# Kernel optimization log

Measured on AMD Instinct MI355X. Metric: run time of the kernel, lower is better.

## Reference

```python
import jax, jax.numpy as jnp
import numpy as np

EPS = 1e-7  # K.epsilon()
ROUTINGS = 3

def squash(v, axis=-1):
    s2 = jnp.sum(jnp.square(v), axis=axis, keepdims=True)
    scale = s2 / (1.0 + s2) / jnp.sqrt(s2 + EPS)
    return scale * v

def setup_inputs() -> dict:
    key = jax.random.key(0)
    k1, k2 = jax.random.split(key)
    B, N, I = 128, 512, 256   # batch, input_num_capsule, input_dim_capsule
    M, D = 32, 16             # num_capsule, dim_capsule
    x = jax.random.normal(k1, (B, N, I), dtype=jnp.float32)
    W = jax.random.normal(k2, (M, N, D, I), dtype=jnp.float32) * 0.05
    return {"x": x, "W": W}

def reference(x, W):
    # x: [B,N,I], W: [M,N,D,I]
    # inputs_hat[b,m,n,d] = sum_i x[b,n,i] * W[m,n,d,i]
    inputs_hat = jnp.einsum('bni,mndi->bmnd', x, W)
    B, M, N, _ = inputs_hat.shape
    b = jnp.zeros((B, M, N), dtype=inputs_hat.dtype)
    outputs = None
    for i in range(ROUTINGS):
        c = jax.nn.softmax(b, axis=1)  # softmax over num_capsule dim (dim=1)
        s = jnp.einsum('bmn,bmnd->bmd', c, inputs_hat)
        outputs = squash(s)
        if i < ROUTINGS - 1:
            b = b + jnp.einsum('bmd,bmnd->bmn', outputs, inputs_hat)
    return outputs
```

## Files before the change

kernel.cpp:

```cpp
#include <hip/hip_runtime.h>
#include <stdint.h>

#define B_ 128
#define N_ 512
#define I_ 256
#define M_ 32
#define D_ 16

typedef __attribute__((ext_vector_type(4))) float f32x4;
typedef __attribute__((ext_vector_type(4))) float float4v;
typedef __attribute__((ext_vector_type(8))) short short8;
typedef __attribute__((ext_vector_type(4))) unsigned int u32x4;
typedef __attribute__((ext_vector_type(4))) unsigned short ushort4v;
typedef unsigned short ushort;

__device__ __forceinline__ float bf2f(ushort u) {
    union { unsigned int i; float f; } v; v.i = ((unsigned int)u) << 16; return v.f;
}
__device__ __forceinline__ ushort f2bf(float f) {
    union { float f; unsigned int i; } v; v.f = f;
    unsigned int r = v.i + 0x7FFFu + ((v.i >> 16) & 1u);
    return (ushort)(r >> 16);
}

__device__ __forceinline__ short8 cvt8(float4v lo, float4v hi) {
    unsigned int u0, u1, u2, u3;
    asm("v_cvt_pk_bf16_f32 %0, %1, %2" : "=v"(u0) : "v"(lo[0]), "v"(lo[1]));
    asm("v_cvt_pk_bf16_f32 %0, %1, %2" : "=v"(u1) : "v"(lo[2]), "v"(lo[3]));
    asm("v_cvt_pk_bf16_f32 %0, %1, %2" : "=v"(u2) : "v"(hi[0]), "v"(hi[1]));
    asm("v_cvt_pk_bf16_f32 %0, %1, %2" : "=v"(u3) : "v"(hi[2]), "v"(hi[3]));
    u32x4 uv = {u0, u1, u2, u3};
    return __builtin_bit_cast(short8, uv);
}

#define GL16(dst, base, imm) \
    asm volatile("global_load_dwordx4 %0, %1, off offset:%2" \
                 : "=&v"(dst) : "v"(base), "n"(imm))

#define VMW(nn) do { \
    asm volatile("s_waitcnt vmcnt(" #nn ")" ::: "memory"); \
    __builtin_amdgcn_sched_barrier(0); \
} while (0)

__global__ __launch_bounds__(512, 4) void hat_gemm(const float* __restrict__ x,
                                                   const float* __restrict__ W,
                                                   ushort* __restrict__ hat) {
    __shared__ ushort As[128 * 256];

    const int bid = blockIdx.x;
    const int n   = (bid & 7) * 64 + (bid >> 3);

    const int tid  = threadIdx.x;
    const int lane = tid & 63;
    const int w    = tid >> 6;
    const int l15  = lane & 15;
    const int kq   = lane >> 4;

    {
        const int row = tid >> 2;
        const int seg = tid & 3;
        const float* xp = x + ((size_t)row * N_ + n) * I_ + seg * 64;
        float4v sv[16];
        #pragma unroll
        for (int j = 0; j < 16; ++j) GL16(sv[j], xp, j * 16);
        VMW(0);
        #pragma unroll
        for (int i = 0; i < 8; ++i) {
            short8 h = cvt8(sv[2 * i], sv[2 * i + 1]);
            const int gsw = ((seg * 8 + i) ^ (row & 15));
            *(short8*)&As[row * 256 + gsw * 8] = h;
        }
    }
    __syncthreads();

    const int abase = l15 * 256;

    #define MF(bb, ks) do { \
        const int gsw_ = (((ks) * 4 + kq) ^ l15) * 8; \
        _Pragma("unroll") \
        for (int a = 0; a < 8; ++a) { \
            short8 af = *(const short8*)&As[abase + a * 4096 + gsw_]; \
            acc[a] = __builtin_amdgcn_mfma_f32_16x16x32_bf16(af, (bb), acc[a], 0, 0, 0); \
        } \
    } while (0)

    #pragma unroll
    for (int mq = 0; mq < 4; ++mq) {
        const int m = w * 4 + mq;
        const float* wm = W + (((size_t)m * N_ + n) * D_ + l15) * I_ + kq * 8;

        f32x4 acc[8];
        #pragma unroll
        for (int a = 0; a < 8; ++a) { f32x4 z = {0.f, 0.f, 0.f, 0.f}; acc[a] = z; }

        float4v L0, H0, L1, H1, L2, H2, L3, H3;
        GL16(L0, wm, 0);   GL16(H0, wm, 16);
        GL16(L1, wm, 128); GL16(H1, wm, 144);
        GL16(L2, wm, 256); GL16(H2, wm, 272);
        GL16(L3, wm, 384); GL16(H3, wm, 400);

        VMW(6); { short8 bb = cvt8(L0, H0); GL16(L0, wm, 512); GL16(H0, wm, 528); MF(bb, 0); }
        VMW(6); { short8 bb = cvt8(L1, H1); GL16(L1, wm, 640); GL16(H1, wm, 656); MF(bb, 1); }
        VMW(6); { short8 bb = cvt8(L2, H2); GL16(L2, wm, 768); GL16(H2, wm, 784); MF(bb, 2); }
        VMW(6); { short8 bb = cvt8(L3, H3); GL16(L3, wm, 896); GL16(H3, wm, 912); MF(bb, 3); }
        VMW(6); { short8 bb = cvt8(L0, H0); MF(bb, 4); }
        VMW(4); { short8 bb = cvt8(L1, H1); MF(bb, 5); }
        VMW(2); { short8 bb = cvt8(L2, H2); MF(bb, 6); }
        VMW(0); { short8 bb = cvt8(L3, H3); MF(bb, 7); }

        #pragma unroll
        for (int a = 0; a < 8; ++a) {
            #pragma unroll
            for (int r = 0; r < 4; ++r) {
                const int brow = a * 16 + kq * 4 + r;
                const size_t idx = (((size_t)brow * M_ + m) * N_ + n) * D_ + l15;
                hat[idx] = f2bf(acc[a][r]);
            }
        }
    }
    #undef MF
}

__global__ __launch_bounds__(512) void routing(const ushort* __restrict__ hat,
                                               float* __restrict__ out) {
    __shared__ float blog[M_][N_];
    __shared__ float cmax[N_];
    __shared__ float rcsum[N_];

    const int b    = blockIdx.x;
    const int tid  = threadIdx.x;
    const int lane = tid & 63;
    const int w    = tid >> 6;

    #pragma unroll
    for (int m = 0; m < M_; ++m) blog[m][tid] = 0.f;
    __syncthreads();

    float ov[4][16];

    for (int it = 0; it < 3; ++it) {
        {
            float mx = -3.4e38f;
            #pragma unroll
            for (int m = 0; m < M_; ++m) mx = fmaxf(mx, blog[m][tid]);
            float s = 0.f;
            #pragma unroll
            for (int m = 0; m < M_; ++m) s += __expf(blog[m][tid] - mx);
            cmax[tid]  = mx;
            rcsum[tid] = 1.f / s;
        }
        __syncthreads();

        float sacc[4][16];
        #pragma unroll
        for (int q = 0; q < 4; ++q)
            #pragma unroll
            for (int dd = 0; dd < 16; ++dd) sacc[q][dd] = 0.f;

        for (int r = 0; r < 8; ++r) {
            const int nn = r * 64 + lane;
            #pragma unroll
            for (int q = 0; q < 4; ++q) {
                const int m = w * 4 + q;
                const float cm = __expf(blog[m][nn] - cmax[nn]) * rcsum[nn];
                const size_t base = (((size_t)b * M_ + m) * N_ + nn) * D_;
                short8 h0 = *(const short8*)(hat + base);
                short8 h1 = *(const short8*)(hat + base + 8);
                #pragma unroll
                for (int dd = 0; dd < 8; ++dd) {
                    sacc[q][dd]     += cm * bf2f((ushort)h0[dd]);
                    sacc[q][8 + dd] += cm * bf2f((ushort)h1[dd]);
                }
            }
        }
        #pragma unroll
        for (int off = 32; off >= 1; off >>= 1) {
            #pragma unroll
            for (int q = 0; q < 4; ++q)
                #pragma unroll
                for (int dd = 0; dd < 16; ++dd)
                    sacc[q][dd] += __shfl_xor(sacc[q][dd], off, 64);
        }
        #pragma unroll
        for (int q = 0; q < 4; ++q) {
            float s2 = 0.f;
            #pragma unroll
            for (int dd = 0; dd < 16; ++dd) s2 += sacc[q][dd] * sacc[q][dd];
            const float scale = s2 / (1.f + s2) / sqrtf(s2 + 1e-7f);
            #pragma unroll
            for (int dd = 0; dd < 16; ++dd) ov[q][dd] = scale * sacc[q][dd];
        }

        if (it < 2) {
            for (int r = 0; r < 8; ++r) {
                const int nn = r * 64 + lane;
                #pragma unroll
                for (int q = 0; q < 4; ++q) {
                    const int m = w * 4 + q;
                    const size_t base = (((size_t)b * M_ + m) * N_ + nn) * D_;
                    short8 h0 = *(const short8*)(hat + base);
                    short8 h1 = *(const short8*)(hat + base + 8);
                    float dot = 0.f;
                    #pragma unroll
                    for (int dd = 0; dd < 8; ++dd) {
                        dot += ov[q][dd]     * bf2f((ushort)h0[dd]);
                        dot += ov[q][8 + dd] * bf2f((ushort)h1[dd]);
                    }
                    blog[m][nn] += dot;
                }
            }
        }
        __syncthreads();
    }

    if (lane == 0) {
        #pragma unroll
        for (int q = 0; q < 4; ++q) {
            const int m = w * 4 + q;
            #pragma unroll
            for (int c4 = 0; c4 < 4; ++c4) {
                float4v v;
                v[0] = ov[q][c4 * 4 + 0];
                v[1] = ov[q][c4 * 4 + 1];
                v[2] = ov[q][c4 * 4 + 2];
                v[3] = ov[q][c4 * 4 + 3];
                *(float4v*)&out[((size_t)b * M_ + m) * D_ + c4 * 4] = v;
            }
        }
    }
}

extern "C" void kernel_launch(void* const* d_in, const int* in_sizes, int n_in,
                              void* d_out, int out_size, void* d_ws, size_t ws_size,
                              hipStream_t stream) {
    const float* x = (const float*)d_in[0];
    const float* W = (const float*)d_in[1];
    ushort* hat = (ushort*)d_ws;
    float* out = (float*)d_out;

    hat_gemm<<<dim3(N_), dim3(512), 0, stream>>>(x, W, hat);
    routing<<<dim3(B_), dim3(512), 0, stream>>>(hat, out);
}
```

Baseline: 173.4 us.

## Prefetch next W tile across m-iterations and fuse routing logit update with softmax pass

In the GEMM, the first W tile loads are issued alongside the x loads, and each following m-iteration's W loads are issued before the current hat stores, so global latency overlaps with store and compute work. In routing, the first iteration uses the known uniform coefficient 1/M instead of a softmax. The logit-update pass and the next weighted-sum pass now share a single read of hat per row chunk, with the softmax computed inline per n after a barrier. This halves hat traffic in the later iterations, at the cost of more barriers inside the loop and higher register pressure from keeping hat fragments live.

Result: no change. 176.4 us (+1.8%).

```diff
diff --git a/kernel.cpp b/kernel.cpp
--- a/kernel.cpp
+++ b/kernel.cpp
@@ -42,6 +42,15 @@
     __builtin_amdgcn_sched_barrier(0); \
 } while (0)
 
+#define SBAR() __builtin_amdgcn_sched_barrier(0)
+
+#define LGKM0_BARRIER() do { \
+    asm volatile("s_waitcnt lgkmcnt(0)" ::: "memory"); \
+    __builtin_amdgcn_sched_barrier(0); \
+    __builtin_amdgcn_s_barrier(); \
+    __builtin_amdgcn_sched_barrier(0); \
+} while (0)
+
 __global__ __launch_bounds__(512, 4) void hat_gemm(const float* __restrict__ x,
                                                    const float* __restrict__ W,
                                                    ushort* __restrict__ hat) {
@@ -56,6 +65,11 @@
     const int l15  = lane & 15;
     const int kq   = lane >> 4;
 
+    const size_t mstride = (size_t)N_ * D_ * I_;
+    const float* wm = W + (((size_t)(w * 4) * N_ + n) * D_ + l15) * I_ + kq * 8;
+
+    float4v L0, H0, L1, H1, L2, H2, L3, H3;
+
     {
         const int row = tid >> 2;
         const int seg = tid & 3;
@@ -63,7 +77,11 @@
         float4v sv[16];
         #pragma unroll
         for (int j = 0; j < 16; ++j) GL16(sv[j], xp, j * 16);
-        VMW(0);
+        GL16(L0, wm, 0);   GL16(H0, wm, 16);
+        GL16(L1, wm, 128); GL16(H1, wm, 144);
+        GL16(L2, wm, 256); GL16(H2, wm, 272);
+        GL16(L3, wm, 384); GL16(H3, wm, 400);
+        VMW(8);
         #pragma unroll
         for (int i = 0; i < 8; ++i) {
             short8 h = cvt8(sv[2 * i], sv[2 * i + 1]);
@@ -71,7 +89,7 @@
             *(short8*)&As[row * 256 + gsw * 8] = h;
         }
     }
-    __syncthreads();
+    LGKM0_BARRIER();
 
     const int abase = l15 * 256;
 
@@ -87,27 +105,35 @@
     #pragma unroll
     for (int mq = 0; mq < 4; ++mq) {
         const int m = w * 4 + mq;
-        const float* wm = W + (((size_t)m * N_ + n) * D_ + l15) * I_ + kq * 8;
 
         f32x4 acc[8];
         #pragma unroll
         for (int a = 0; a < 8; ++a) { f32x4 z = {0.f, 0.f, 0.f, 0.f}; acc[a] = z; }
 
-        float4v L0, H0, L1, H1, L2, H2, L3, H3;
-        GL16(L0, wm, 0);   GL16(H0, wm, 16);
-        GL16(L1, wm, 128); GL16(H1, wm, 144);
-        GL16(L2, wm, 256); GL16(H2, wm, 272);
-        GL16(L3, wm, 384); GL16(H3, wm, 400);
-
-        VMW(6); { short8 bb = cvt8(L0, H0); GL16(L0, wm, 512); GL16(H0, wm, 528); MF(bb, 0); }
-        VMW(6); { short8 bb = cvt8(L1, H1); GL16(L1, wm, 640); GL16(H1, wm, 656); MF(bb, 1); }
-        VMW(6); { short8 bb = cvt8(L2, H2); GL16(L2, wm, 768); GL16(H2, wm, 784); MF(bb, 2); }
-        VMW(6); { short8 bb = cvt8(L3, H3); GL16(L3, wm, 896); GL16(H3, wm, 912); MF(bb, 3); }
-        VMW(6); { short8 bb = cvt8(L0, H0); MF(bb, 4); }
-        VMW(4); { short8 bb = cvt8(L1, H1); MF(bb, 5); }
-        VMW(2); { short8 bb = cvt8(L2, H2); MF(bb, 6); }
-        VMW(0); { short8 bb = cvt8(L3, H3); MF(bb, 7); }
-
+        if (mq == 0) {
+            VMW(6);  { short8 bb = cvt8(L0, H0); GL16(L0, wm, 512); GL16(H0, wm, 528); MF(bb, 0); }
+            VMW(6);  { short8 bb = cvt8(L1, H1); GL16(L1, wm, 640); GL16(H1, wm, 656); MF(bb, 1); }
+            VMW(6);  { short8 bb = cvt8(L2, H2); GL16(L2, wm, 768); GL16(H2, wm, 784); MF(bb, 2); }
+            VMW(6);  { short8 bb = cvt8(L3, H3); GL16(L3, wm, 896); GL16(H3, wm, 912); MF(bb, 3); }
+        } else {
+            VMW(38); { short8 bb = cvt8(L0, H0); GL16(L0, wm, 512); GL16(H0, wm, 528); MF(bb, 0); }
+            VMW(38); { short8 bb = cvt8(L1, H1); GL16(L1, wm, 640); GL16(H1, wm, 656); MF(bb, 1); }
+            VMW(38); { short8 bb = cvt8(L2, H2); GL16(L2, wm, 768); GL16(H2, wm, 784); MF(bb, 2); }
+            VMW(38); { short8 bb = cvt8(L3, H3); GL16(L3, wm, 896); GL16(H3, wm, 912); MF(bb, 3); }
+        }
+        VMW(6);  { short8 bb = cvt8(L0, H0); MF(bb, 4); }
+        VMW(4);  { short8 bb = cvt8(L1, H1); MF(bb, 5); }
+        VMW(2);  { short8 bb = cvt8(L2, H2); MF(bb, 6); }
+        VMW(0);  { short8 bb = cvt8(L3, H3); MF(bb, 7); }
+
+        if (mq < 3) {
+            wm += mstride;
+            GL16(L0, wm, 0);   GL16(H0, wm, 16);
+            GL16(L1, wm, 128); GL16(H1, wm, 144);
+            GL16(L2, wm, 256); GL16(H2, wm, 272);
+            GL16(L3, wm, 384); GL16(H3, wm, 400);
+            SBAR();
+        }
         #pragma unroll
         for (int a = 0; a < 8; ++a) {
             #pragma unroll
@@ -117,15 +143,15 @@
                 hat[idx] = f2bf(acc[a][r]);
             }
         }
+        SBAR();
     }
     #undef MF
-}
-
-__global__ __launch_bounds__(512) void routing(const ushort* __restrict__ hat,
-                                               float* __restrict__ out) {
+    VMW(0);
+}
+
+__global__ __launch_bounds__(512, 1) void routing(const ushort* __restrict__ hat,
+                                                  float* __restrict__ out) {
     __shared__ float blog[M_][N_];
-    __shared__ float cmax[N_];
-    __shared__ float rcsum[N_];
 
     const int b    = blockIdx.x;
     const int tid  = threadIdx.x;
@@ -136,22 +162,52 @@
     for (int m = 0; m < M_; ++m) blog[m][tid] = 0.f;
     __syncthreads();
 
-    float ov[4][16];
-
-    for (int it = 0; it < 3; ++it) {
-        {
-            float mx = -3.4e38f;
-            #pragma unroll
-            for (int m = 0; m < M_; ++m) mx = fmaxf(mx, blog[m][tid]);
-            float s = 0.f;
-            #pragma unroll
-            for (int m = 0; m < M_; ++m) s += __expf(blog[m][tid] - mx);
-            cmax[tid]  = mx;
-            rcsum[tid] = 1.f / s;
-        }
-        __syncthreads();
-
-        float sacc[4][16];
+    float ov[4][16], sacc[4][16];
+
+    #define REDUCE_SQUASH() do { \
+        _Pragma("unroll") \
+        for (int off = 32; off >= 1; off >>= 1) { \
+            _Pragma("unroll") \
+            for (int q = 0; q < 4; ++q) \
+                _Pragma("unroll") \
+                for (int dd = 0; dd < 16; ++dd) \
+                    sacc[q][dd] += __shfl_xor(sacc[q][dd], off, 64); \
+        } \
+        _Pragma("unroll") \
+        for (int q = 0; q < 4; ++q) { \
+            float s2 = 0.f; \
+            _Pragma("unroll") \
+            for (int dd = 0; dd < 16; ++dd) s2 += sacc[q][dd] * sacc[q][dd]; \
+            const float scale = s2 / (1.f + s2) / sqrtf(s2 + 1e-7f); \
+            _Pragma("unroll") \
+            for (int dd = 0; dd < 16; ++dd) ov[q][dd] = scale * sacc[q][dd]; \
+        } \
+    } while (0)
+
+    #pragma unroll
+    for (int q = 0; q < 4; ++q)
+        #pragma unroll
+        for (int dd = 0; dd < 16; ++dd) sacc[q][dd] = 0.f;
+
+    for (int r = 0; r < 8; ++r) {
+        const int nn = r * 64 + lane;
+        #pragma unroll
+        for (int q = 0; q < 4; ++q) {
+            const int m = w * 4 + q;
+            const size_t base = (((size_t)b * M_ + m) * N_ + nn) * D_;
+            short8 h0 = *(const short8*)(hat + base);
+            short8 h1 = *(const short8*)(hat + base + 8);
+            const float cm = 0.03125f;
+            #pragma unroll
+            for (int dd = 0; dd < 8; ++dd) {
+                sacc[q][dd]     += cm * bf2f((ushort)h0[dd]);
+                sacc[q][8 + dd] += cm * bf2f((ushort)h1[dd]);
+            }
+        }
+    }
+    REDUCE_SQUASH();
+
+    for (int t = 0; t < 2; ++t) {
         #pragma unroll
         for (int q = 0; q < 4; ++q)
             #pragma unroll
@@ -159,59 +215,42 @@
 
         for (int r = 0; r < 8; ++r) {
             const int nn = r * 64 + lane;
+            short8 hh0[4], hh1[4];
             #pragma unroll
             for (int q = 0; q < 4; ++q) {
                 const int m = w * 4 + q;
-                const float cm = __expf(blog[m][nn] - cmax[nn]) * rcsum[nn];
                 const size_t base = (((size_t)b * M_ + m) * N_ + nn) * D_;
-                short8 h0 = *(const short8*)(hat + base);
-                short8 h1 = *(const short8*)(hat + base + 8);
+                hh0[q] = *(const short8*)(hat + base);
+                hh1[q] = *(const short8*)(hat + base + 8);
+                float dot = 0.f;
                 #pragma unroll
                 for (int dd = 0; dd < 8; ++dd) {
-                    sacc[q][dd]     += cm * bf2f((ushort)h0[dd]);
-                    sacc[q][8 + dd] += cm * bf2f((ushort)h1[dd]);
+                    dot += ov[q][dd]     * bf2f((ushort)hh0[q][dd]);
+                    dot += ov[q][8 + dd] * bf2f((ushort)hh1[q][dd]);
                 }
-            }
-        }
-        #pragma unroll
-        for (int off = 32; off >= 1; off >>= 1) {
-            #pragma unroll
-            for (int q = 0; q < 4; ++q)
+                blog[m][nn] += dot;
+            }
+            __syncthreads();
+            float mx = -3.4e38f;
+            #pragma unroll
+            for (int mm = 0; mm < M_; ++mm) mx = fmaxf(mx, blog[mm][nn]);
+            float ss = 0.f;
+            #pragma unroll
+            for (int mm = 0; mm < M_; ++mm) ss += __expf(blog[mm][nn] - mx);
+            const float rs = 1.f / ss;
+            #pragma unroll
+            for (int q = 0; q < 4; ++q) {
+                const float cm = __expf(blog[w * 4 + q][nn] - mx) * rs;
                 #pragma unroll
-                for (int dd = 0; dd < 16; ++dd)
-                    sacc[q][dd] += __shfl_xor(sacc[q][dd], off, 64);
-        }
-        #pragma unroll
-        for (int q = 0; q < 4; ++q) {
-            float s2 = 0.f;
-            #pragma unroll
-            for (int dd = 0; dd < 16; ++dd) s2 += sacc[q][dd] * sacc[q][dd];
-            const float scale = s2 / (1.f + s2) / sqrtf(s2 + 1e-7f);
-            #pragma unroll
-            for (int dd = 0; dd < 16; ++dd) ov[q][dd] = scale * sacc[q][dd];
-        }
-
-        if (it < 2) {
-            for (int r = 0; r < 8; ++r) {
-                const int nn = r * 64 + lane;
-                #pragma unroll
-                for (int q = 0; q < 4; ++q) {
-                    const int m = w * 4 + q;
-                    const size_t base = (((size_t)b * M_ + m) * N_ + nn) * D_;
-                    short8 h0 = *(const short8*)(hat + base);
-                    short8 h1 = *(const short8*)(hat + base + 8);
-                    float dot = 0.f;
-                    #pragma unroll
-                    for (int dd = 0; dd < 8; ++dd) {
-                        dot += ov[q][dd]     * bf2f((ushort)h0[dd]);
-                        dot += ov[q][8 + dd] * bf2f((ushort)h1[dd]);
-                    }
-                    blog[m][nn] += dot;
+                for (int dd = 0; dd < 8; ++dd) {
+                    sacc[q][dd]     += cm * bf2f((ushort)hh0[q][dd]);
+                    sacc[q][8 + dd] += cm * bf2f((ushort)hh1[q][dd]);
                 }
             }
         }
-        __syncthreads();
-    }
+        REDUCE_SQUASH();
+    }
+    #undef REDUCE_SQUASH
 
     if (lane == 0) {
         #pragma unroll
```
